# Performance work log

Hardware: AMD Instinct MI355X
Metric: run time of the kernel (lower is better)

Reference implementation:

```python
import jax, jax.numpy as jnp
import numpy as np

N = 100000      # nodes (single node type)
R = 4           # relations
E = 800000      # edges per relation (avg in-degree ~32)
D_IN, D_H, D_OUT = 256, 64, 16


def setup_inputs() -> dict:
    key = jax.random.key(0)
    ks = jax.random.split(key, 9)
    x = jax.random.normal(ks[0], (N, D_IN), dtype=jnp.float32)
    src = jax.random.randint(ks[1], (R, E), 0, N, dtype=jnp.int32)
    dst = jax.random.randint(ks[2], (R, E), 0, N, dtype=jnp.int32)
    s_in = 1.0 / np.sqrt(D_IN)
    s_h = 1.0 / np.sqrt(D_H)
    W1 = jax.random.normal(ks[3], (R, D_IN, D_H), dtype=jnp.float32) * s_in
    L1w = jax.random.normal(ks[4], (D_IN, D_H), dtype=jnp.float32) * s_in
    L1b = jnp.zeros((D_H,), dtype=jnp.float32)
    W2 = jax.random.normal(ks[5], (R, D_H, D_OUT), dtype=jnp.float32) * s_h
    L2w = jax.random.normal(ks[6], (D_H, D_OUT), dtype=jnp.float32) * s_h
    L2b = jnp.zeros((D_OUT,), dtype=jnp.float32)
    return {"x": x, "src": src, "dst": dst, "W1": W1, "L1w": L1w,
            "L1b": L1b, "W2": W2, "L2w": L2w, "L2b": L2b}


def _rel_graph_conv(h, src, dst, W):
    """Per-relation GEMM + gather + scatter-add + right-normalize, summed over relations.
    h: [N, d_in]; src/dst: [R, E]; W: [R, d_in, d_out] -> [N, d_out]
    """
    hw = jnp.einsum('nd,rdh->rnh', h, W)  # transform first (d_out small), then gather

    def agg(hr, s, d):
        deg = jax.ops.segment_sum(jnp.ones((E,), hr.dtype), d, num_segments=N)
        msg = jax.ops.segment_sum(hr[s], d, num_segments=N)  # [N, d_out]
        return msg / jnp.maximum(deg, 1.0)[:, None]          # norm='right'

    return jnp.sum(jax.vmap(agg)(hw, src, dst), axis=0)


def reference(x, src, dst, W1, L1w, L1b, W2, L2w, L2b):
    # Layer 1: relation conv + self-loop linear + ReLU (dropout = eval/identity)
    h = _rel_graph_conv(x, src, dst, W1) + x @ L1w + L1b
    h = jax.nn.relu(h)
    # Layer 2: no activation
    out = _rel_graph_conv(h, src, dst, W2) + h @ L2w + L2b
    return out
```

## Files before the change

kernel.cpp:

```cpp
#include <hip/hip_runtime.h>


constexpr int NN = 100000, RR = 4, EE = 800000;
constexpr int RE = RR * EE;
constexpr int NBKT = (NN + 63) / 64;
constexpr int BCAP = 3072;
constexpr int NG1 = (NN + 63) / 64;
constexpr int CHUNK = 8192;
constexpr int NB = (RE + CHUNK - 1) / CHUNK;
constexpr int EPT = CHUNK / 512;

typedef short bf16x8 __attribute__((ext_vector_type(8)));
typedef float f32x4 __attribute__((ext_vector_type(4)));

__device__ inline unsigned short f2bf(float f) {
  unsigned u = __float_as_uint(f);
  u += 0x7FFF + ((u >> 16) & 1);
  return (unsigned short)(u >> 16);
}
__device__ inline float bf2f(unsigned short s) {
  return __uint_as_float(((unsigned)s) << 16);
}

__global__ __launch_bounds__(256) void prep_w_kernel(const float* __restrict__ W1,
                                                     const float* __restrict__ L1w,
                                                     const float* __restrict__ W2,
                                                     const float* __restrict__ L2w,
                                                     unsigned short* __restrict__ BT1sw,
                                                     unsigned short* __restrict__ BT2) {
  int idx = blockIdx.x * 256 + threadIdx.x;
  if (idx < 320 * 256) {
    int n = idx >> 8, k = idx & 255;
    float v = (n < 256) ? W1[((size_t)((n >> 6) * 256 + k)) * 64 + (n & 63)]
                        : L1w[(size_t)k * 64 + (n - 256)];
    int kc = k >> 6, c = (k & 63) >> 3, e = k & 7;
    int byteoff = kc * 40960 + ((n * 128 + c * 16) ^ ((n & 7) << 4)) + e * 2;
    *(unsigned short*)((char*)BT1sw + byteoff) = f2bf(v);
  } else {
    int j = idx - 320 * 256;
    if (j < 80 * 64) {
      int n = j >> 6, k = j & 63;
      float v = (n < 64) ? W2[((size_t)((n >> 4) * 64 + k)) * 16 + (n & 15)]
                         : L2w[(size_t)k * 16 + (n - 64)];
      BT2[j] = f2bf(v);
    }
  }
}

__global__ __launch_bounds__(512) void fused1_kernel(const float* __restrict__ x,
                                                     const unsigned short* __restrict__ BT1sw,
                                                     const float* __restrict__ L1b,
                                                     const int* __restrict__ src,
                                                     const int* __restrict__ dst,
                                                     int* __restrict__ gcur,
                                                     int* __restrict__ binned,
                                                     unsigned short* __restrict__ hwcat,
                                                     unsigned short* __restrict__ h) {
  __shared__ char lds[49152];
  const int bid = blockIdx.x;
  const int t = threadIdx.x;
  const bool is_bin = (bid % 5 == 0) && (bid / 5 < NB);

  if (is_bin) {
    int* hist = (int*)lds;
    int* base = hist + NBKT;
    for (int k = t; k < NBKT; k += 512) hist[k] = 0;
    __syncthreads();
    const int e0 = (bid / 5) * CHUNK + t;
    int dl[EPT], sl[EPT];
#pragma unroll
    for (int i = 0; i < EPT; ++i) {
      int fl = e0 + i * 512;
      dl[i] = -1;
      if (fl < RE) {
        dl[i] = dst[fl];
        sl[i] = src[fl];
        atomicAdd(&hist[dl[i] >> 6], 1);
      }
    }
    __syncthreads();
    for (int k = t; k < NBKT; k += 512) {
      int hv = hist[k];
      base[k] = hv ? atomicAdd(&gcur[k], hv) : 0;
      hist[k] = 0;
    }
    __syncthreads();
#pragma unroll
    for (int i = 0; i < EPT; ++i) {
      if (dl[i] < 0) continue;
      int fl = e0 + i * 512;
      int r = fl / EE;
      int b = dl[i] >> 6;
      int off = atomicAdd(&hist[b], 1);
      int p = base[b] + off;
      if (p < BCAP) binned[(size_t)b * BCAP + p] = (sl[i] << 2) | r | ((dl[i] & 63) << 19);
    }
    return;
  }

  int nbins = (bid + 4) / 5;
  if (nbins > NB) nbins = NB;
  const int m0 = (bid - nbins) * 64;
  char* Al = lds;
  char* Bl = lds + 8192;
  const int wid = t >> 6, lane = t & 63;
  const int wm = wid >> 2, wn = wid & 3;
  const int l15 = lane & 15, g = lane >> 4;

  f32x4 acc[2][5];
#pragma unroll
  for (int i = 0; i < 2; ++i)
#pragma unroll
    for (int j = 0; j < 5; ++j) acc[i][j] = (f32x4){0.f, 0.f, 0.f, 0.f};

  const int row0 = t >> 4, kq0 = (t & 15) * 4;
  const int row1 = (t + 512) >> 4, kq1 = ((t + 512) & 15) * 4;
  const int rg0 = m0 + row0, rg1 = m0 + row1;
  const float4 z4 = make_float4(0.f, 0.f, 0.f, 0.f);

  float4 a0 = (rg0 < NN) ? *(const float4*)(x + (size_t)rg0 * 256 + kq0) : z4;
  float4 a1 = (rg1 < NN) ? *(const float4*)(x + (size_t)rg1 * 256 + kq1) : z4;

  for (int kc = 0; kc < 4; ++kc) {
    if (kc) __syncthreads();
    {
      const char* gB = (const char*)BT1sw + kc * 40960;
#pragma unroll
      for (int it = 0; it < 5; ++it) {
        int sl5 = (it * 8 + wid) * 1024;
        __builtin_amdgcn_global_load_lds((const unsigned int*)(gB + sl5 + lane * 16),
                                         (unsigned int*)(Bl + sl5), 16, 0, 0);
      }
    }
    {
      ushort4 p0 = {f2bf(a0.x), f2bf(a0.y), f2bf(a0.z), f2bf(a0.w)};
      int wb0 = ((row0 * 64 + kq0) * 2) ^ ((row0 & 7) << 4);
      *(ushort4*)(Al + wb0) = p0;
      ushort4 p1 = {f2bf(a1.x), f2bf(a1.y), f2bf(a1.z), f2bf(a1.w)};
      int wb1 = ((row1 * 64 + kq1) * 2) ^ ((row1 & 7) << 4);
      *(ushort4*)(Al + wb1) = p1;
    }
    __syncthreads();
    if (kc < 3) {
      a0 = (rg0 < NN) ? *(const float4*)(x + (size_t)rg0 * 256 + (kc + 1) * 64 + kq0) : z4;
      a1 = (rg1 < NN) ? *(const float4*)(x + (size_t)rg1 * 256 + (kc + 1) * 64 + kq1) : z4;
    }
#pragma unroll
    for (int ks = 0; ks < 2; ++ks) {
      bf16x8 af[2], bfr[5];
#pragma unroll
      for (int mi = 0; mi < 2; ++mi) {
        int row = wm * 32 + mi * 16 + l15;
        int byte = ((row * 64 + ks * 32 + g * 8) * 2) ^ ((row & 7) << 4);
        af[mi] = *(const bf16x8*)(Al + byte);
      }
#pragma unroll
      for (int ni = 0; ni < 5; ++ni) {
        int n = wn * 80 + ni * 16 + l15;
        int byte = ((n * 64 + ks * 32 + g * 8) * 2) ^ ((n & 7) << 4);
        bfr[ni] = *(const bf16x8*)(Bl + byte);
      }
#pragma unroll
      for (int mi = 0; mi < 2; ++mi)
#pragma unroll
        for (int ni = 0; ni < 5; ++ni)
          acc[mi][ni] = __builtin_amdgcn_mfma_f32_16x16x32_bf16(af[mi], bfr[ni], acc[mi][ni], 0, 0, 0);
    }
  }
#pragma unroll
  for (int mi = 0; mi < 2; ++mi) {
    int rbase = m0 + wm * 32 + mi * 16 + 4 * g;
#pragma unroll
    for (int ni = 0; ni < 5; ++ni) {
      int n0 = wn * 80 + ni * 16;
      int n = n0 + l15;
#pragma unroll
      for (int e = 0; e < 4; ++e) {
        int row = rbase + e;
        if (row >= NN) continue;
        float v = acc[mi][ni][e];
        if (n0 < 256) hwcat[(size_t)row * 256 + n] = f2bf(v);
        else h[(size_t)row * 64 + (n - 256)] = f2bf(v + L1b[n - 256]);
      }
    }
  }
}

__global__ __launch_bounds__(256) void pull1_kernel(const unsigned short* __restrict__ h,
                                                    const unsigned short* __restrict__ hwcat,
                                                    int* __restrict__ binned,
                                                    const int* __restrict__ gcur,
                                                    const unsigned short* __restrict__ BT2,
                                                    const float* __restrict__ L2b,
                                                    unsigned* __restrict__ hdrG,
                                                    float* __restrict__ winvG,
                                                    unsigned short* __restrict__ hw2,
                                                    float* __restrict__ out) {
  __shared__ int csr[BCAP];
  __shared__ int cnt[256];
  __shared__ int off[256];
  __shared__ float winv[256];
  __shared__ int tot[64];
  __shared__ int wsum[4];
  __shared__ char Al[64 * 64 * 2];
  const int t = threadIdx.x, bkt = blockIdx.x;
  const int wid = t >> 6, lane = t & 63;
  const int l15 = lane & 15, g = lane >> 4;

  int count = gcur[bkt];
  if (count > BCAP) count = BCAP;
  const int* edges = binned + (size_t)bkt * BCAP;

  cnt[t] = 0;
  __syncthreads();
  for (int i = t; i < count; i += 256) {
    int w = edges[i];
    atomicAdd(&cnt[((w >> 19) & 63) * 4 + (w & 3)], 1);
  }
  __syncthreads();
  int v = cnt[t];
  int xs = v;
#pragma unroll
  for (int d = 1; d < 64; d <<= 1) {
    int y = __shfl_up(xs, d);
    if (lane >= d) xs += y;
  }
  if (lane == 63) wsum[wid] = xs;
  __syncthreads();
  int add = 0;
#pragma unroll
  for (int w2 = 0; w2 < 4; ++w2)
    if (w2 < wid) add += wsum[w2];
  int excl = xs + add - v;
  winv[t] = 1.0f / (float)(v > 1 ? v : 1);
  off[t] = excl;
  cnt[t] = excl;
  __syncthreads();
  if (t < 64) tot[t] = ((t == 63) ? count : off[(t + 1) * 4]) - off[t * 4];
  for (int i = t; i < count; i += 256) {
    int w = edges[i];
    int k = ((w >> 19) & 63) * 4 + (w & 3);
    int p = atomicAdd(&cnt[k], 1);
    csr[p] = w & 0x7FFFF;
  }
  __syncthreads();

  for (int i = t; i < count; i += 256) binned[(size_t)bkt * BCAP + i] = csr[i];
  winvG[bkt * 256 + t] = winv[t];
  if (t < 64) hdrG[bkt * 64 + t] = (unsigned)off[t * 4] | ((unsigned)tot[t] << 16);

  const int slot = lane >> 3, cpart = lane & 7;
  for (int ii = 0; ii < 16; ++ii) {
    int nloc = wid * 16 + ii;
    int beg = off[nloc * 4];
    int total = tot[nloc];
    float acc[8] = {0.f, 0.f, 0.f, 0.f, 0.f, 0.f, 0.f, 0.f};
    for (int p0 = 0; p0 < total; p0 += 8) {
      int j = p0 + slot;
      bool pr = j < total;
      int key = pr ? csr[beg + j] : 0;
      float wv = pr ? winv[nloc * 4 + (key & 3)] : 0.f;
      uint4 u = *(const uint4*)(hwcat + (size_t)key * 64 + cpart * 8);
#pragma unroll
      for (int q = 0; q < 4; ++q) {
        unsigned uu = (&u.x)[q];
        acc[q * 2]     = fmaf(wv, bf2f((unsigned short)(uu & 0xffffu)), acc[q * 2]);
        acc[q * 2 + 1] = fmaf(wv, bf2f((unsigned short)(uu >> 16)), acc[q * 2 + 1]);
      }
    }
#pragma unroll
    for (int m = 8; m <= 32; m <<= 1)
#pragma unroll
      for (int q = 0; q < 8; ++q) acc[q] += __shfl_xor(acc[q], m);
    if (slot == 0) {
      int gn = bkt * 64 + nloc;
      unsigned pk[4];
      uint4 hu = make_uint4(0, 0, 0, 0);
      if (gn < NN) hu = *(const uint4*)(h + (size_t)gn * 64 + cpart * 8);
#pragma unroll
      for (int q = 0; q < 4; ++q) {
        unsigned a = (&hu.x)[q];
        float v0 = acc[q * 2]     + bf2f((unsigned short)(a & 0xffffu));
        float v1 = acc[q * 2 + 1] + bf2f((unsigned short)(a >> 16));
        pk[q] = (unsigned)f2bf(fmaxf(v0, 0.f)) | ((unsigned)f2bf(fmaxf(v1, 0.f)) << 16);
      }
      int wb = ((nloc * 64 + cpart * 8) * 2) ^ ((nloc & 7) << 4);
      *(uint4*)(Al + wb) = make_uint4(pk[0], pk[1], pk[2], pk[3]);
    }
  }
  __syncthreads();

  char* Bl = (char*)csr;
#pragma unroll
  for (int it = 0; it < 3; ++it) {
    int fl = t + 256 * it;
    if (fl < 640) {
      int n = fl >> 3, i8 = (fl & 7) * 8;
      uint4 u = *(const uint4*)(BT2 + (size_t)n * 64 + i8);
      int wb = ((n * 64 + i8) * 2) ^ ((n & 7) << 4);
      *(uint4*)(Bl + wb) = u;
    }
  }
  __syncthreads();

  f32x4 acc2[5];
#pragma unroll
  for (int j = 0; j < 5; ++j) acc2[j] = (f32x4){0.f, 0.f, 0.f, 0.f};
#pragma unroll
  for (int ks = 0; ks < 2; ++ks) {
    int ra = wid * 16 + l15;
    int byte = ((ra * 64 + ks * 32 + g * 8) * 2) ^ ((ra & 7) << 4);
    bf16x8 af = *(const bf16x8*)(Al + byte);
#pragma unroll
    for (int ni = 0; ni < 5; ++ni) {
      int n = ni * 16 + l15;
      int nb = ((n * 64 + ks * 32 + g * 8) * 2) ^ ((n & 7) << 4);
      bf16x8 bfr = *(const bf16x8*)(Bl + nb);
      acc2[ni] = __builtin_amdgcn_mfma_f32_16x16x32_bf16(af, bfr, acc2[ni], 0, 0, 0);
    }
  }
  int rb = wid * 16 + 4 * g;
#pragma unroll
  for (int ni = 0; ni < 5; ++ni) {
    int n0 = ni * 16;
    int n = n0 + l15;
#pragma unroll
    for (int e = 0; e < 4; ++e) {
      int gno = bkt * 64 + rb + e;
      if (gno >= NN) continue;
      float vv = acc2[ni][e];
      if (n0 < 64) hw2[(size_t)gno * 64 + n] = f2bf(vv);
      else out[(size_t)gno * 16 + (n - 64)] = vv + L2b[n - 64];
    }
  }
}

__global__ __launch_bounds__(256) void pull2_kernel(const unsigned short* __restrict__ hw2,
                                                    const int* __restrict__ binned,
                                                    const int* __restrict__ gcur,
                                                    const unsigned* __restrict__ hdrG,
                                                    const float* __restrict__ winvG,
                                                    float* __restrict__ out) {
  __shared__ int csr[BCAP];
  __shared__ float winvL[256];
  __shared__ int begL[64], totL[64];
  __shared__ float ot[64][16];
  const int t = threadIdx.x, bkt = blockIdx.x;
  const int wid = t >> 6, lane = t & 63;

  int count = gcur[bkt];
  if (count > BCAP) count = BCAP;
  for (int i = t; i < count; i += 256) csr[i] = binned[(size_t)bkt * BCAP + i];
  winvL[t] = winvG[bkt * 256 + t];
  if (t < 64) {
    unsigned hd = hdrG[bkt * 64 + t];
    begL[t] = hd & 0xffff;
    totL[t] = hd >> 16;
  }
  __syncthreads();

  const int slot = lane >> 2, cpart = lane & 3;
  for (int ii = 0; ii < 16; ++ii) {
    int nloc = wid * 16 + ii;
    int beg = begL[nloc];
    int total = totL[nloc];
    float acc[4] = {0.f, 0.f, 0.f, 0.f};
    for (int p0 = 0; p0 < total; p0 += 16) {
      int j = p0 + slot;
      bool pr = j < total;
      int key = pr ? csr[beg + j] : 0;
      float wv = pr ? winvL[nloc * 4 + (key & 3)] : 0.f;
      uint2 u = *(const uint2*)(hw2 + (size_t)key * 16 + cpart * 4);
      acc[0] = fmaf(wv, bf2f((unsigned short)(u.x & 0xffffu)), acc[0]);
      acc[1] = fmaf(wv, bf2f((unsigned short)(u.x >> 16)), acc[1]);
      acc[2] = fmaf(wv, bf2f((unsigned short)(u.y & 0xffffu)), acc[2]);
      acc[3] = fmaf(wv, bf2f((unsigned short)(u.y >> 16)), acc[3]);
    }
#pragma unroll
    for (int m = 4; m <= 32; m <<= 1)
#pragma unroll
      for (int q = 0; q < 4; ++q) acc[q] += __shfl_xor(acc[q], m);
    if (slot == 0)
      *(float4*)&ot[nloc][cpart * 4] = make_float4(acc[0], acc[1], acc[2], acc[3]);
  }
  __syncthreads();

  int row = t >> 2, q = t & 3;
  int gn = bkt * 64 + row;
  if (gn < NN) {
    float4 o = *(float4*)(out + (size_t)gn * 16 + q * 4);
    float4 a = *(float4*)&ot[row][q * 4];
    o.x += a.x; o.y += a.y; o.z += a.z; o.w += a.w;
    *(float4*)(out + (size_t)gn * 16 + q * 4) = o;
  }
}

extern "C" void kernel_launch(void* const* d_in, const int* in_sizes, int n_in,
                              void* d_out, int out_size, void* d_ws, size_t ws_size,
                              hipStream_t stream) {
  const float* x   = (const float*)d_in[0];
  const int*   src = (const int*)d_in[1];
  const int*   dst = (const int*)d_in[2];
  const float* W1  = (const float*)d_in[3];
  const float* L1w = (const float*)d_in[4];
  const float* L1b = (const float*)d_in[5];
  const float* W2  = (const float*)d_in[6];
  const float* L2w = (const float*)d_in[7];
  const float* L2b = (const float*)d_in[8];
  float* out = (float*)d_out;

  char* p = (char*)d_ws;
  int* binned = (int*)p;                      p += (size_t)NBKT * BCAP * 4;
  int* gcur   = (int*)p;                      p += 8192;
  unsigned short* hwcat = (unsigned short*)p; p += (size_t)NN * 256 * 2;
  unsigned short* h = (unsigned short*)p;     p += (size_t)NN * 64 * 2;
  unsigned short* hw2 = (unsigned short*)p;   p += (size_t)NN * 64 * 2;
  unsigned short* BT1sw = (unsigned short*)p; p += 4 * 40960;
  unsigned short* BT2 = (unsigned short*)p;   p += 80 * 64 * 2;
  unsigned* hdrG = (unsigned*)p;              p += (size_t)NBKT * 64 * 4;
  float* winvG = (float*)p;                   p += (size_t)NBKT * 256 * 4;
  if ((size_t)(p - (char*)d_ws) > ws_size) return;

  hipMemsetAsync(gcur, 0, NBKT * 4, stream);
  prep_w_kernel<<<(320 * 256 + 80 * 64 + 255) / 256, 256, 0, stream>>>(W1, L1w, W2, L2w, BT1sw, BT2);
  fused1_kernel<<<NG1 + NB, 512, 0, stream>>>(x, BT1sw, L1b, src, dst, gcur, binned, hwcat, h);
  pull1_kernel<<<NBKT, 256, 0, stream>>>(h, hwcat, binned, gcur, BT2, L2b, hdrG, winvG, hw2, out);
  pull2_kernel<<<NBKT, 256, 0, stream>>>(hw2, binned, gcur, hdrG, winvG, out);
}
```

Before: 235.5 us.

## Restructure layer-1 GEMM to keep full-K weight slice resident in LDS

Each GEMM block now owns one of four 80-column output slices and loads that slice for the full K=256 into LDS once. It then loops over four 64-row M tiles, reading x straight from global into MFMA operand registers. Blocks shrink to 256 threads, and the binning blocks are adjusted to the same width with twice the edges per thread. This drops the per-k-chunk B reloads and the A staging through LDS. The cost is that x is read by four column-slice blocks instead of once, which depends on L2 reuse across adjacent blocks, and per-wave A loads have no latency hiding.

```diff
diff --git a/kernel.cpp b/kernel.cpp
--- a/kernel.cpp
+++ b/kernel.cpp
@@ -6,9 +6,11 @@
 constexpr int NBKT = (NN + 63) / 64;
 constexpr int BCAP = 3072;
 constexpr int NG1 = (NN + 63) / 64;
+constexpr int NMG = 391;
+constexpr int NGEMM = 4 * NMG;
 constexpr int CHUNK = 8192;
 constexpr int NB = (RE + CHUNK - 1) / CHUNK;
-constexpr int EPT = CHUNK / 512;
+constexpr int EPT = CHUNK / 256;
 
 typedef short bf16x8 __attribute__((ext_vector_type(8)));
 typedef float f32x4 __attribute__((ext_vector_type(4)));
@@ -26,16 +28,14 @@
                                                      const float* __restrict__ L1w,
                                                      const float* __restrict__ W2,
                                                      const float* __restrict__ L2w,
-                                                     unsigned short* __restrict__ BT1sw,
+                                                     unsigned short* __restrict__ BT1,
                                                      unsigned short* __restrict__ BT2) {
   int idx = blockIdx.x * 256 + threadIdx.x;
   if (idx < 320 * 256) {
     int n = idx >> 8, k = idx & 255;
     float v = (n < 256) ? W1[((size_t)((n >> 6) * 256 + k)) * 64 + (n & 63)]
                         : L1w[(size_t)k * 64 + (n - 256)];
-    int kc = k >> 6, c = (k & 63) >> 3, e = k & 7;
-    int byteoff = kc * 40960 + ((n * 128 + c * 16) ^ ((n & 7) << 4)) + e * 2;
-    *(unsigned short*)((char*)BT1sw + byteoff) = f2bf(v);
+    BT1[idx] = f2bf(v);
   } else {
     int j = idx - 320 * 256;
     if (j < 80 * 64) {
@@ -47,8 +47,8 @@
   }
 }
 
-__global__ __launch_bounds__(512) void fused1_kernel(const float* __restrict__ x,
-                                                     const unsigned short* __restrict__ BT1sw,
+__global__ __launch_bounds__(256) void fused1_kernel(const float* __restrict__ x,
+                                                     const unsigned short* __restrict__ BT1,
                                                      const float* __restrict__ L1b,
                                                      const int* __restrict__ src,
                                                      const int* __restrict__ dst,
@@ -56,7 +56,7 @@
                                                      int* __restrict__ binned,
                                                      unsigned short* __restrict__ hwcat,
                                                      unsigned short* __restrict__ h) {
-  __shared__ char lds[49152];
+  __shared__ char lds[40960];
   const int bid = blockIdx.x;
   const int t = threadIdx.x;
   const bool is_bin = (bid % 5 == 0) && (bid / 5 < NB);
@@ -64,13 +64,13 @@
   if (is_bin) {
     int* hist = (int*)lds;
     int* base = hist + NBKT;
-    for (int k = t; k < NBKT; k += 512) hist[k] = 0;
+    for (int k = t; k < NBKT; k += 256) hist[k] = 0;
     __syncthreads();
     const int e0 = (bid / 5) * CHUNK + t;
     int dl[EPT], sl[EPT];
 #pragma unroll
     for (int i = 0; i < EPT; ++i) {
-      int fl = e0 + i * 512;
+      int fl = e0 + i * 256;
       dl[i] = -1;
       if (fl < RE) {
         dl[i] = dst[fl];
@@ -79,7 +79,7 @@
       }
     }
     __syncthreads();
-    for (int k = t; k < NBKT; k += 512) {
+    for (int k = t; k < NBKT; k += 256) {
       int hv = hist[k];
       base[k] = hv ? atomicAdd(&gcur[k], hv) : 0;
       hist[k] = 0;
@@ -88,7 +88,7 @@
 #pragma unroll
     for (int i = 0; i < EPT; ++i) {
       if (dl[i] < 0) continue;
-      int fl = e0 + i * 512;
+      int fl = e0 + i * 256;
       int r = fl / EE;
       int b = dl[i] >> 6;
       int off = atomicAdd(&hist[b], 1);
@@ -100,87 +100,63 @@
 
   int nbins = (bid + 4) / 5;
   if (nbins > NB) nbins = NB;
-  const int m0 = (bid - nbins) * 64;
-  char* Al = lds;
-  char* Bl = lds + 8192;
+  const int gid = bid - nbins;
+  const int q = gid & 3;
+  const int mg = gid >> 2;
+  char* Bl = lds;
   const int wid = t >> 6, lane = t & 63;
-  const int wm = wid >> 2, wn = wid & 3;
   const int l15 = lane & 15, g = lane >> 4;
 
-  f32x4 acc[2][5];
-#pragma unroll
-  for (int i = 0; i < 2; ++i)
-#pragma unroll
-    for (int j = 0; j < 5; ++j) acc[i][j] = (f32x4){0.f, 0.f, 0.f, 0.f};
-
-  const int row0 = t >> 4, kq0 = (t & 15) * 4;
-  const int row1 = (t + 512) >> 4, kq1 = ((t + 512) & 15) * 4;
-  const int rg0 = m0 + row0, rg1 = m0 + row1;
+#pragma unroll
+  for (int it = 0; it < 10; ++it) {
+    int fl = t + 256 * it;
+    int ln = fl >> 5, c = fl & 31;
+    uint4 u = *(const uint4*)(BT1 + (size_t)(q * 80 + ln) * 256 + c * 8);
+    int off = (ln * 512 + c * 16) ^ ((ln & 7) << 4);
+    *(uint4*)(Bl + off) = u;
+  }
+  __syncthreads();
+
   const float4 z4 = make_float4(0.f, 0.f, 0.f, 0.f);
-
-  float4 a0 = (rg0 < NN) ? *(const float4*)(x + (size_t)rg0 * 256 + kq0) : z4;
-  float4 a1 = (rg1 < NN) ? *(const float4*)(x + (size_t)rg1 * 256 + kq1) : z4;
-
-  for (int kc = 0; kc < 4; ++kc) {
-    if (kc) __syncthreads();
-    {
-      const char* gB = (const char*)BT1sw + kc * 40960;
-#pragma unroll
-      for (int it = 0; it < 5; ++it) {
-        int sl5 = (it * 8 + wid) * 1024;
-        __builtin_amdgcn_global_load_lds((const unsigned int*)(gB + sl5 + lane * 16),
-                                         (unsigned int*)(Bl + sl5), 16, 0, 0);
+  for (int j = 0; j < 4; ++j) {
+    int mt = mg * 4 + j;
+    if (mt >= NG1) break;
+    int m0 = mt * 64;
+    int row = m0 + wid * 16 + l15;
+    bool rok = row < NN;
+    f32x4 acc[5];
+#pragma unroll
+    for (int f = 0; f < 5; ++f) acc[f] = (f32x4){0.f, 0.f, 0.f, 0.f};
+#pragma unroll
+    for (int ks = 0; ks < 8; ++ks) {
+      const float* ap = x + (size_t)row * 256 + ks * 32 + g * 8;
+      float4 u0 = rok ? *(const float4*)ap : z4;
+      float4 u1 = rok ? *(const float4*)(ap + 4) : z4;
+      bf16x8 af;
+      af[0] = (short)f2bf(u0.x); af[1] = (short)f2bf(u0.y);
+      af[2] = (short)f2bf(u0.z); af[3] = (short)f2bf(u0.w);
+      af[4] = (short)f2bf(u1.x); af[5] = (short)f2bf(u1.y);
+      af[6] = (short)f2bf(u1.z); af[7] = (short)f2bf(u1.w);
+#pragma unroll
+      for (int f = 0; f < 5; ++f) {
+        int ln = f * 16 + l15;
+        int off = (ln * 512 + ks * 64 + g * 16) ^ ((ln & 7) << 4);
+        bf16x8 bfr = *(const bf16x8*)(Bl + off);
+        acc[f] = __builtin_amdgcn_mfma_f32_16x16x32_bf16(af, bfr, acc[f], 0, 0, 0);
       }
     }
-    {
-      ushort4 p0 = {f2bf(a0.x), f2bf(a0.y), f2bf(a0.z), f2bf(a0.w)};
-      int wb0 = ((row0 * 64 + kq0) * 2) ^ ((row0 & 7) << 4);
-      *(ushort4*)(Al + wb0) = p0;
-      ushort4 p1 = {f2bf(a1.x), f2bf(a1.y), f2bf(a1.z), f2bf(a1.w)};
-      int wb1 = ((row1 * 64 + kq1) * 2) ^ ((row1 & 7) << 4);
-      *(ushort4*)(Al + wb1) = p1;
-    }
-    __syncthreads();
-    if (kc < 3) {
-      a0 = (rg0 < NN) ? *(const float4*)(x + (size_t)rg0 * 256 + (kc + 1) * 64 + kq0) : z4;
-      a1 = (rg1 < NN) ? *(const float4*)(x + (size_t)rg1 * 256 + (kc + 1) * 64 + kq1) : z4;
-    }
-#pragma unroll
-    for (int ks = 0; ks < 2; ++ks) {
-      bf16x8 af[2], bfr[5];
-#pragma unroll
-      for (int mi = 0; mi < 2; ++mi) {
-        int row = wm * 32 + mi * 16 + l15;
-        int byte = ((row * 64 + ks * 32 + g * 8) * 2) ^ ((row & 7) << 4);
-        af[mi] = *(const bf16x8*)(Al + byte);
-      }
-#pragma unroll
-      for (int ni = 0; ni < 5; ++ni) {
-        int n = wn * 80 + ni * 16 + l15;
-        int byte = ((n * 64 + ks * 32 + g * 8) * 2) ^ ((n & 7) << 4);
-        bfr[ni] = *(const bf16x8*)(Bl + byte);
-      }
-#pragma unroll
-      for (int mi = 0; mi < 2; ++mi)
-#pragma unroll
-        for (int ni = 0; ni < 5; ++ni)
-          acc[mi][ni] = __builtin_amdgcn_mfma_f32_16x16x32_bf16(af[mi], bfr[ni], acc[mi][ni], 0, 0, 0);
-    }
-  }
-#pragma unroll
-  for (int mi = 0; mi < 2; ++mi) {
-    int rbase = m0 + wm * 32 + mi * 16 + 4 * g;
-#pragma unroll
-    for (int ni = 0; ni < 5; ++ni) {
-      int n0 = wn * 80 + ni * 16;
+    int rbase = m0 + wid * 16 + 4 * g;
+#pragma unroll
+    for (int f = 0; f < 5; ++f) {
+      int n0 = q * 80 + f * 16;
       int n = n0 + l15;
 #pragma unroll
       for (int e = 0; e < 4; ++e) {
-        int row = rbase + e;
-        if (row >= NN) continue;
-        float v = acc[mi][ni][e];
-        if (n0 < 256) hwcat[(size_t)row * 256 + n] = f2bf(v);
-        else h[(size_t)row * 64 + (n - 256)] = f2bf(v + L1b[n - 256]);
+        int rw = rbase + e;
+        if (rw >= NN) continue;
+        float v = acc[f][e];
+        if (n0 < 256) hwcat[(size_t)rw * 256 + n] = f2bf(v);
+        else h[(size_t)rw * 64 + (n - 256)] = f2bf(v + L1b[n - 256]);
       }
     }
   }
@@ -415,15 +391,15 @@
   unsigned short* hwcat = (unsigned short*)p; p += (size_t)NN * 256 * 2;
   unsigned short* h = (unsigned short*)p;     p += (size_t)NN * 64 * 2;
   unsigned short* hw2 = (unsigned short*)p;   p += (size_t)NN * 64 * 2;
-  unsigned short* BT1sw = (unsigned short*)p; p += 4 * 40960;
+  unsigned short* BT1 = (unsigned short*)p;   p += 320 * 256 * 2;
   unsigned short* BT2 = (unsigned short*)p;   p += 80 * 64 * 2;
   unsigned* hdrG = (unsigned*)p;              p += (size_t)NBKT * 64 * 4;
   float* winvG = (float*)p;                   p += (size_t)NBKT * 256 * 4;
   if ((size_t)(p - (char*)d_ws) > ws_size) return;
 
   hipMemsetAsync(gcur, 0, NBKT * 4, stream);
-  prep_w_kernel<<<(320 * 256 + 80 * 64 + 255) / 256, 256, 0, stream>>>(W1, L1w, W2, L2w, BT1sw, BT2);
-  fused1_kernel<<<NG1 + NB, 512, 0, stream>>>(x, BT1sw, L1b, src, dst, gcur, binned, hwcat, h);
+  prep_w_kernel<<<(320 * 256 + 80 * 64 + 255) / 256, 256, 0, stream>>>(W1, L1w, W2, L2w, BT1, BT2);
+  fused1_kernel<<<NGEMM + NB, 256, 0, stream>>>(x, BT1, L1b, src, dst, gcur, binned, hwcat, h);
   pull1_kernel<<<NBKT, 256, 0, stream>>>(h, hwcat, binned, gcur, BT2, L2b, hdrG, winvG, hw2, out);
   pull2_kernel<<<NBKT, 256, 0, stream>>>(hw2, binned, gcur, hdrG, winvG, out);
 }
```

Result: slower. 386.6 us (+64.1%).
